# Kernel tuning notes

Measured on AMD Instinct MI355X. Metric: run time of the kernel, lower is better.

The kernel has to match this reference:

```python
import jax, jax.numpy as jnp
import numpy as np

V, E, HID, L = 32000, 2048, 8192, 4
H, KV, DK, DH = 16, 4, 128, 128
SEQ, WINDOW = 2048, 1024
EPS = 1e-5


def rms_norm(x):
    return x * jax.lax.rsqrt(jnp.mean(x * x, axis=-1, keepdims=True) + EPS)


def rope_buffers(seq_len, key_size):
    half = key_size // 2
    offset = jnp.arange(key_size) % half
    scales = jnp.power(10000.0, -2.0 / key_size * offset.astype(jnp.float32))
    angles = jnp.arange(seq_len, dtype=jnp.float32)[:, None] * scales[None, :]  # [S, DK]
    cos = jnp.cos(angles)
    sin = jnp.sin(angles)
    sin = sin.at[:, :half].multiply(-1.0)
    return cos, sin


def rotate(f, cos, sin):
    # f: [B, heads, S, DK]; cos/sin: [S, DK]
    half = DK // 2
    swapped = jnp.concatenate([f[..., half:], f[..., :half]], axis=-1)
    return cos * f + sin * swapped


def sliding_window_attention(q, k, v, window):
    # q: [B,H,S,DK], k: [B,KV,S,DK], v: [B,KV,S,DH]; GQA broadcast
    B, _, S, _ = q.shape
    G = H // KV
    qg = q.reshape(B, KV, G, S, DK)
    scores = jnp.einsum('bkgqd,bkjd->bkgqj', qg, k) / jnp.sqrt(jnp.asarray(DK, q.dtype))
    i = jnp.arange(S)[:, None]
    j = jnp.arange(S)[None, :]
    mask = (j <= i) & (i - j < window)
    scores = jnp.where(mask, scores, jnp.asarray(-1e9, scores.dtype))
    probs = jax.nn.softmax(scores, axis=-1)
    out = jnp.einsum('bkgqj,bkjd->bkgqd', probs, v)
    return out.reshape(B, H, S, DH)


def setup_inputs() -> dict:
    key = jax.random.key(0)
    ks = jax.random.split(key, 9)
    s = lambda k, shape, fan: jax.random.normal(k, shape, jnp.float32) / np.sqrt(fan)
    return {
        'tokens': jax.random.randint(ks[0], (1, SEQ), 0, V),
        'table': jax.random.normal(ks[1], (V, E), jnp.float32) * 0.02,
        'wq': s(ks[2], (L, E, H * DK), E),
        'wk': s(ks[3], (L, E, KV * DK), E),
        'wv': s(ks[4], (L, E, KV * DH), E),
        'wo': s(ks[5], (L, H * DH, E), H * DH),
        'w_up': s(ks[6], (L, E, 2 * HID), E),
        'w_down': s(ks[7], (L, HID, E), HID),
        'w_vocab': s(ks[8], (E, V), E),
    }


def reference(tokens, table, wq, wk, wv, wo, w_up, w_down, w_vocab):
    B, S = tokens.shape
    table = table.at[0].set(0.0)  # forward zeroes row 0 each call
    cos, sin = rope_buffers(S, DK)
    x = table[tokens]  # [B, S, E]
    for l in range(L):
        # --- self attention ---
        n = rms_norm(x)
        q = (n @ wq[l]).reshape(B, S, H, DK).transpose(0, 2, 1, 3)
        k = (n @ wk[l]).reshape(B, S, KV, DK).transpose(0, 2, 1, 3)
        v = (n @ wv[l]).reshape(B, S, KV, DH).transpose(0, 2, 1, 3)
        q = rotate(q, cos, sin)
        k = rotate(k, cos, sin)
        attn = sliding_window_attention(q, k, v, WINDOW)
        attn = attn.transpose(0, 2, 1, 3).reshape(B, S, H * DH)
        x = x + attn @ wo[l]
        # --- SwiGLU FFN ---
        n = rms_norm(x)
        gu = n @ w_up[l]
        gate, up = gu[..., :HID], gu[..., HID:]
        x = x + (up * jax.nn.silu(gate)) @ w_down[l]
    x = rms_norm(x)
    logits = x @ w_vocab  # [B, S, V]
    return logits
```

## Files before the change

### kernel.cpp

```cpp
#include <hip/hip_runtime.h>
#include <cstdint>

typedef unsigned short bf16u;
typedef __attribute__((ext_vector_type(8))) short short8;
typedef __attribute__((ext_vector_type(4))) float f32x4;

#define SEQ   2048
#define EMB   2048
#define NHEAD 16
#define NKV   4
#define DKH   128
#define HIDN  8192
#define NVOC  32000
#define NLAY  4
#define WIN   1024
#define QKV_N 3072

__device__ __forceinline__ bf16u f2bf(float f) {
  union { float f; uint32_t u; } v; v.f = f;
  uint32_t r = v.u + 0x7FFFu + ((v.u >> 16) & 1u);
  return (bf16u)(r >> 16);
}

__device__ __forceinline__ void gl2lds16(const void* g, void* l) {
  __builtin_amdgcn_global_load_lds(
      (const __attribute__((address_space(1))) void*)g,
      (__attribute__((address_space(3))) void*)l, 16, 0, 0);
}

__global__ __launch_bounds__(256) void embed_kernel(const int* __restrict__ tokens,
                                                    const float* __restrict__ table,
                                                    float* __restrict__ x) {
  int s = blockIdx.x;
  int tok = tokens[s];
  int i0 = threadIdx.x * 8;
  float4 a = {0,0,0,0}, b = {0,0,0,0};
  if (tok != 0) {
    const float* src = table + (size_t)tok * EMB;
    a = *(const float4*)(src + i0);
    b = *(const float4*)(src + i0 + 4);
  }
  *(float4*)(x + (size_t)s * EMB + i0) = a;
  *(float4*)(x + (size_t)s * EMB + i0 + 4) = b;
}

__global__ __launch_bounds__(256) void rmsnorm_kernel(const float* __restrict__ x,
                                                      bf16u* __restrict__ out) {
  int s = blockIdx.x;
  const float* row = x + (size_t)s * EMB;
  int i0 = threadIdx.x * 8;
  float4 a = *(const float4*)(row + i0);
  float4 b = *(const float4*)(row + i0 + 4);
  float ss = a.x*a.x + a.y*a.y + a.z*a.z + a.w*a.w
           + b.x*b.x + b.y*b.y + b.z*b.z + b.w*b.w;
  #pragma unroll
  for (int off = 1; off < 64; off <<= 1) ss += __shfl_xor(ss, off);
  __shared__ float red[4];
  if ((threadIdx.x & 63) == 0) red[threadIdx.x >> 6] = ss;
  __syncthreads();
  float scale = rsqrtf((red[0] + red[1] + red[2] + red[3]) * (1.0f / EMB) + 1e-5f);
  float v[8] = {a.x, a.y, a.z, a.w, b.x, b.y, b.z, b.w};
  short8 o;
  #pragma unroll
  for (int j = 0; j < 8; ++j) o[j] = (short)f2bf(v[j] * scale);
  *(short8*)(out + (size_t)s * EMB + i0) = o;
}

__global__ __launch_bounds__(256) void transp_kernel(const float* __restrict__ in,
                                                     bf16u* __restrict__ out,
                                                     int R, int C) {
  __shared__ float tile[32][33];
  int c0 = blockIdx.x * 32, r0 = blockIdx.y * 32;
  int tx = threadIdx.x & 31, ty = threadIdx.x >> 5;
  #pragma unroll
  for (int i = 0; i < 4; ++i)
    tile[ty + i * 8][tx] = in[(size_t)(r0 + ty + i * 8) * C + c0 + tx];
  __syncthreads();
  #pragma unroll
  for (int i = 0; i < 4; ++i)
    out[(size_t)(c0 + ty + i * 8) * R + r0 + tx] = f2bf(tile[tx][ty + i * 8]);
}

__global__ __launch_bounds__(256) void rope_kernel(const float* __restrict__ qkv,
                                                   bf16u* __restrict__ out, int col0) {
  int idx = blockIdx.x * 256 + threadIdx.x;
  int d = idx & 63;
  int s = (idx >> 6) & (SEQ - 1);
  int h = idx >> 17;
  const float* row = qkv + (size_t)s * QKV_N + col0 + h * DKH;
  float ang = (float)s * __powf(10000.0f, -(float)d * (1.0f / 64.0f));
  float si, c;
  sincosf(ang, &si, &c);
  float f0 = row[d], f1 = row[d + 64];
  bf16u* orow = out + ((size_t)h * SEQ + s) * DKH;
  orow[d]      = f2bf(c * f0 - si * f1);
  orow[d + 64] = f2bf(c * f1 + si * f0);
}

__global__ __launch_bounds__(256) void vconv_kernel(const float* __restrict__ qkv,
                                                    bf16u* __restrict__ vout) {
  int idx = blockIdx.x * 256 + threadIdx.x;
  int d = idx & 127;
  int kv = (idx >> 7) & 3;
  int s = idx >> 9;
  vout[((size_t)kv * SEQ + s) * DKH + d] = f2bf(qkv[(size_t)s * QKV_N + 2560 + kv * DKH + d]);
}

__global__ __launch_bounds__(256) void swiglu_kernel(const float* __restrict__ gu,
                                                     bf16u* __restrict__ h) {
  size_t idx = (size_t)blockIdx.x * 256 + threadIdx.x;
  int s = (int)(idx >> 13);
  int j = (int)(idx & 8191);
  float g = gu[(size_t)s * 16384 + j];
  float u = gu[(size_t)s * 16384 + 8192 + j];
  float sil = g / (1.0f + __expf(-g));
  h[idx] = f2bf(u * sil);
}

__global__ __launch_bounds__(256) void reduce4_kernel(float* __restrict__ x,
                                                      const float* __restrict__ p) {
  size_t i = ((size_t)blockIdx.x * 256 + threadIdx.x) * 4;
  const size_t MN = (size_t)SEQ * EMB;
  float4 a = *(const float4*)(x + i);
  float4 b0 = *(const float4*)(p + i);
  float4 b1 = *(const float4*)(p + i + MN);
  float4 b2 = *(const float4*)(p + i + 2 * MN);
  float4 b3 = *(const float4*)(p + i + 3 * MN);
  a.x += b0.x + b1.x + b2.x + b3.x;
  a.y += b0.y + b1.y + b2.y + b3.y;
  a.z += b0.z + b1.z + b2.z + b3.z;
  a.w += b0.w + b1.w + b2.w + b3.w;
  *(float4*)(x + i) = a;
}

template <int MODE>
__global__ __launch_bounds__(256) void gemm_kernel(const bf16u* __restrict__ A,
                                                   const bf16u* __restrict__ Bt,
                                                   void* __restrict__ C,
                                                   int M, int N, int K) {
  __shared__ __align__(16) char lds[2][2][8192];

  int nx = gridDim.x, ny = gridDim.y;
  int nwg = nx * ny;
  int orig = blockIdx.y * nx + blockIdx.x;
  int q = nwg >> 3, r = nwg & 7;
  int xcd = orig & 7, loc = orig >> 3;
  int id = (xcd < r ? xcd * (q + 1) : r * (q + 1) + (xcd - r) * q) + loc;
  int bx = id / ny, by = id - bx * ny;
  int n0 = bx * 128, m0 = by * 128;

  int t = threadIdx.x;
  int w = t >> 6, l = t & 63;
  int wm = (w >> 1) * 64, wn = (w & 1) * 64;
  int l15 = l & 15, l4 = l >> 4;

  int srow = w * 16 + (l >> 2);
  int scol = (l & 3) * 8;

  f32x4 acc[4][4] = {};

  auto stage = [&](int buf, int k0) {
    #pragma unroll
    for (int i = 0; i < 2; ++i) {
      gl2lds16(A  + (size_t)(m0 + i * 64 + srow) * K + k0 + scol,
               &lds[buf][0][i * 4096 + w * 1024]);
      gl2lds16(Bt + (size_t)(n0 + i * 64 + srow) * K + k0 + scol,
               &lds[buf][1][i * 4096 + w * 1024]);
    }
  };

  auto compute = [&](int buf) {
    short8 af[4], bfr[4];
    #pragma unroll
    for (int i = 0; i < 4; ++i) {
      af[i]  = *(const short8*)(&lds[buf][0][((wm + i * 16 + l15) * 32 + l4 * 8) * 2]);
      bfr[i] = *(const short8*)(&lds[buf][1][((wn + i * 16 + l15) * 32 + l4 * 8) * 2]);
    }
    #pragma unroll
    for (int i = 0; i < 4; ++i)
      #pragma unroll
      for (int j = 0; j < 4; ++j)
        acc[i][j] = __builtin_amdgcn_mfma_f32_16x16x32_bf16(af[i], bfr[j], acc[i][j], 0, 0, 0);
  };

  int nt = K >> 5;
  int cur = 0;
  stage(0, 0);
  __syncthreads();
  for (int tt = 0; tt < nt; ++tt) {
    if (tt + 1 < nt) stage(cur ^ 1, (tt + 1) * 32);
    compute(cur);
    __syncthreads();
    cur ^= 1;
  }

  #pragma unroll
  for (int i = 0; i < 4; ++i)
    #pragma unroll
    for (int j = 0; j < 4; ++j) {
      int col = n0 + wn + j * 16 + l15;
      #pragma unroll
      for (int rr = 0; rr < 4; ++rr) {
        int row = m0 + wm + i * 16 + l4 * 4 + rr;
        float v = acc[i][j][rr];
        if (MODE == 0) {
          ((bf16u*)C)[(size_t)row * N + col] = f2bf(v);
        } else if (MODE == 1) {
          float* p = (float*)C + (size_t)row * N + col;
          *p += v;
        } else {
          ((float*)C)[(size_t)row * N + col] = v;
        }
      }
    }
}

__device__ __forceinline__ void stage_half(const bf16u* __restrict__ p, int ld,
                                           int row0, int k0, char* slotBase, int t) {
  int r  = t >> 3, c8 = t & 7;
  int cs = (c8 ^ (r & 7)) << 3;
  gl2lds16(p + (size_t)(row0 + r) * ld + k0 + cs, slotBase + t * 16);
  gl2lds16(p + (size_t)(row0 + 64 + r) * ld + k0 + cs, slotBase + 8192 + t * 16);
}

template<int KK>
__device__ __forceinline__ short8 read_frag(const char* slot, int row, int l4) {
  int kc = KK * 4 + l4;
  return *(const short8*)(slot + row * 128 + ((kc ^ (row & 7)) << 4));
}

template<int NH>
__device__ __forceinline__ void mfma_quad(f32x4 (&acc)[8][4], const short8 (&a)[8],
                                          short8 b0, short8 b1) {
  __builtin_amdgcn_s_setprio(1);
  #pragma unroll
  for (int mi = 0; mi < 8; ++mi) {
    acc[mi][NH * 2]     = __builtin_amdgcn_mfma_f32_16x16x32_bf16(a[mi], b0, acc[mi][NH * 2], 0, 0, 0);
    acc[mi][NH * 2 + 1] = __builtin_amdgcn_mfma_f32_16x16x32_bf16(a[mi], b1, acc[mi][NH * 2 + 1], 0, 0, 0);
  }
  __builtin_amdgcn_s_setprio(0);
}

template <int MODE>
__global__ __launch_bounds__(512) void gemm256_kernel(const bf16u* __restrict__ A,
                                                      const bf16u* __restrict__ Bt,
                                                      void* __restrict__ C,
                                                      int M, int N, int K, int ldk) {
  __shared__ __align__(16) char lds[131072];

  int koff = blockIdx.z * K;
  A  += koff;
  Bt += koff;
  float* Cz = (float*)C + (size_t)blockIdx.z * M * N;

  int nx = gridDim.x, ny = gridDim.y;
  int nwg = nx * ny;
  int orig = blockIdx.y * nx + blockIdx.x;
  int q8 = nwg >> 3, r8 = nwg & 7;
  int xcd = orig & 7, loc = orig >> 3;
  int id = (xcd < r8 ? xcd * (q8 + 1) : r8 * (q8 + 1) + (xcd - r8) * q8) + loc;
  int bx = id / ny, by = id - bx * ny;
  int n0 = bx * 256, m0 = by * 256;

  int t = threadIdx.x;
  int wid = t >> 6, lane = t & 63;
  int wr = wid >> 2, wc = wid & 3, bh = wc >> 1;
  int l15 = lane & 15, l4 = lane >> 4;

  char* AS0 = lds;              char* AS1 = lds + 16384;
  char* AS2 = lds + 32768;      char* AS3 = lds + 49152;
  char* BS0 = lds + 65536;      char* BS1 = lds + 81920;
  char* BS2 = lds + 98304;      char* BS3 = lds + 114688;

  const char* ASe = lds + wr * 16384;
  const char* ASo = ASe + 32768;
  const char* BSe = lds + 65536 + bh * 16384;
  const char* BSo = BSe + 32768;

  int brow = (wc & 1) * 64;

  f32x4 acc[8][4] = {};
  short8 a[8];
  short8 b0, b1;

  int NT = K >> 6;
  int NI = NT >> 1;

  stage_half(A,  ldk, m0,       0,  AS0, t);
  stage_half(A,  ldk, m0 + 128, 0,  AS1, t);
  stage_half(Bt, ldk, n0,       0,  BS0, t);
  stage_half(Bt, ldk, n0 + 128, 0,  BS1, t);
  stage_half(A,  ldk, m0,       64, AS2, t);
  asm volatile("s_waitcnt vmcnt(2)" ::: "memory");
  __builtin_amdgcn_s_barrier();
  __builtin_amdgcn_sched_barrier(0);

  for (int I = 0; I < NI; ++I) {
    int t0k = I * 128;
    int t1k = t0k + 64;
    bool notlast = (I + 1 < NI);

    #pragma unroll
    for (int mi = 0; mi < 8; ++mi) a[mi] = read_frag<0>(ASe, mi * 16 + l15, l4);
    b0 = read_frag<0>(BSe, brow + l15, l4);
    b1 = read_frag<0>(BSe, brow + 16 + l15, l4);
    stage_half(A, ldk, m0 + 128, t1k, AS3, t);
    __builtin_amdgcn_s_barrier();
    mfma_quad<0>(acc, a, b0, b1);
    __builtin_amdgcn_s_barrier();

    b0 = read_frag<0>(BSe, brow + 32 + l15, l4);
    b1 = read_frag<0>(BSe, brow + 48 + l15, l4);
    stage_half(Bt, ldk, n0, t1k, BS2, t);
    __builtin_amdgcn_s_barrier();
    mfma_quad<1>(acc, a, b0, b1);
    __builtin_amdgcn_s_barrier();

    #pragma unroll
    for (int mi = 0; mi < 8; ++mi) a[mi] = read_frag<1>(ASe, mi * 16 + l15, l4);
    b0 = read_frag<1>(BSe, brow + l15, l4);
    b1 = read_frag<1>(BSe, brow + 16 + l15, l4);
    stage_half(Bt, ldk, n0 + 128, t1k, BS3, t);
    __builtin_amdgcn_s_barrier();
    mfma_quad<0>(acc, a, b0, b1);
    __builtin_amdgcn_s_barrier();

    b0 = read_frag<1>(BSe, brow + 32 + l15, l4);
    b1 = read_frag<1>(BSe, brow + 48 + l15, l4);
    if (notlast) stage_half(A, ldk, m0, t0k + 128, AS0, t);
    if (notlast) { asm volatile("s_waitcnt vmcnt(2)" ::: "memory"); }
    else         { asm volatile("s_waitcnt vmcnt(0)" ::: "memory"); }
    __builtin_amdgcn_s_barrier();
    __builtin_amdgcn_sched_barrier(0);
    mfma_quad<1>(acc, a, b0, b1);
    __builtin_amdgcn_s_barrier();

    #pragma unroll
    for (int mi = 0; mi < 8; ++mi) a[mi] = read_frag<0>(ASo, mi * 16 + l15, l4);
    b0 = read_frag<0>(BSo, brow + l15, l4);
    b1 = read_frag<0>(BSo, brow + 16 + l15, l4);
    if (notlast) stage_half(A, ldk, m0 + 128, t0k + 128, AS1, t);
    __builtin_amdgcn_s_barrier();
    mfma_quad<0>(acc, a, b0, b1);
    __builtin_amdgcn_s_barrier();

    b0 = read_frag<0>(BSo, brow + 32 + l15, l4);
    b1 = read_frag<0>(BSo, brow + 48 + l15, l4);
    if (notlast) stage_half(Bt, ldk, n0, t0k + 128, BS0, t);
    __builtin_amdgcn_s_barrier();
    mfma_quad<1>(acc, a, b0, b1);
    __builtin_amdgcn_s_barrier();

    #pragma unroll
    for (int mi = 0; mi < 8; ++mi) a[mi] = read_frag<1>(ASo, mi * 16 + l15, l4);
    b0 = read_frag<1>(BSo, brow + l15, l4);
    b1 = read_frag<1>(BSo, brow + 16 + l15, l4);
    if (notlast) stage_half(Bt, ldk, n0 + 128, t0k + 128, BS1, t);
    __builtin_amdgcn_s_barrier();
    mfma_quad<0>(acc, a, b0, b1);
    __builtin_amdgcn_s_barrier();

    b0 = read_frag<1>(BSo, brow + 32 + l15, l4);
    b1 = read_frag<1>(BSo, brow + 48 + l15, l4);
    if (notlast) {
      stage_half(A, ldk, m0, t0k + 192, AS2, t);
      asm volatile("s_waitcnt vmcnt(2)" ::: "memory");
    }
    __builtin_amdgcn_s_barrier();
    __builtin_amdgcn_sched_barrier(0);
    mfma_quad<1>(acc, a, b0, b1);
    __builtin_amdgcn_s_barrier();
  }

  #pragma unroll
  for (int mi = 0; mi < 8; ++mi)
    #pragma unroll
    for (int ni = 0; ni < 4; ++ni) {
      int col = n0 + wc * 64 + ni * 16 + l15;
      #pragma unroll
      for (int rr = 0; rr < 4; ++rr) {
        int row = m0 + wr * 128 + mi * 16 + l4 * 4 + rr;
        float v = acc[mi][ni][rr];
        if (MODE == 0) {
          ((bf16u*)C)[(size_t)row * N + col] = f2bf(v);
        } else if (MODE == 1) {
          float* p = (float*)C + (size_t)row * N + col;
          *p += v;
        } else {
          Cz[(size_t)row * N + col] = v;
        }
      }
    }
}

__global__ __launch_bounds__(256) void attn_kernel(const bf16u* __restrict__ q_bf,
                                                   const bf16u* __restrict__ k_bf,
                                                   const bf16u* __restrict__ v_bf,
                                                   bf16u* __restrict__ attn_out) {
  int h = blockIdx.y;
  int q0 = blockIdx.x * 64;
  int kvh = h >> 2;
  const bf16u* Kp = k_bf + (size_t)kvh * SEQ * DKH;
  const bf16u* Vp = v_bf + (size_t)kvh * SEQ * DKH;

  __shared__ __align__(16) char  Klds[32 * 128 * 2];
  __shared__ __align__(16) bf16u Vlds[128][40];
  __shared__ __align__(16) bf16u Plds[4][16][40];

  int t = threadIdx.x, wave = t >> 6, lane = t & 63;
  int l15 = lane & 15, l4 = lane >> 4;
  int qrow0 = q0 + wave * 16;

  short8 qf[4];
  #pragma unroll
  for (int ks = 0; ks < 4; ++ks)
    qf[ks] = *(const short8*)(q_bf + ((size_t)h * SEQ + qrow0 + l15) * DKH + ks * 32 + l4 * 8);

  f32x4 o[8] = {};
  float m[4], lsum[4];
  #pragma unroll
  for (int r = 0; r < 4; ++r) { m[r] = -INFINITY; lsum[r] = 0.0f; }

  int jstart = q0 >= (WIN - 1) ? ((q0 - (WIN - 1)) & ~31) : 0;

  for (int j0 = jstart; j0 < q0 + 64; j0 += 32) {
    __syncthreads();
    #pragma unroll
    for (int i = 0; i < 2; ++i) {
      int c = t + i * 256;
      int key = c >> 4, cc = c & 15;
      int off = key * 256 + cc * 16; off ^= (key & 7) << 4;
      *(short8*)(Klds + off) = *(const short8*)(Kp + (size_t)(j0 + key) * DKH + cc * 8);
    }
    {
      int key = t >> 3, d0 = (t & 7) * 16;
      const bf16u* src = Vp + (size_t)(j0 + key) * DKH + d0;
      #pragma unroll
      for (int i = 0; i < 16; ++i) Vlds[d0 + i][key] = src[i];
    }
    __syncthreads();

    f32x4 sacc[2] = {};
    #pragma unroll
    for (int nt = 0; nt < 2; ++nt) {
      int key = nt * 16 + l15;
      #pragma unroll
      for (int ks = 0; ks < 4; ++ks) {
        int off = key * 256 + ks * 64 + l4 * 16; off ^= (key & 7) << 4;
        short8 kf = *(short8*)(Klds + off);
        sacc[nt] = __builtin_amdgcn_mfma_f32_16x16x32_bf16(qf[ks], kf, sacc[nt], 0, 0, 0);
      }
    }

    float sv[2][4];
    #pragma unroll
    for (int nt = 0; nt < 2; ++nt) {
      int jk = j0 + nt * 16 + l15;
      #pragma unroll
      for (int r = 0; r < 4; ++r) {
        int iq = qrow0 + l4 * 4 + r;
        float s = sacc[nt][r] * 0.08838834764831845f;
        bool valid = (jk <= iq) && (iq - jk < WIN);
        sv[nt][r] = valid ? s : -1e9f;
      }
    }

    float p[2][4];
    #pragma unroll
    for (int r = 0; r < 4; ++r) {
      float mx = fmaxf(sv[0][r], sv[1][r]);
      #pragma unroll
      for (int off = 1; off < 16; off <<= 1) mx = fmaxf(mx, __shfl_xor(mx, off));
      float mn = fmaxf(m[r], mx);
      float alpha = __expf(m[r] - mn);
      p[0][r] = __expf(sv[0][r] - mn);
      p[1][r] = __expf(sv[1][r] - mn);
      float ps = p[0][r] + p[1][r];
      #pragma unroll
      for (int off = 1; off < 16; off <<= 1) ps += __shfl_xor(ps, off);
      lsum[r] = lsum[r] * alpha + ps;
      m[r] = mn;
      #pragma unroll
      for (int d = 0; d < 8; ++d) o[d][r] *= alpha;
    }

    #pragma unroll
    for (int nt = 0; nt < 2; ++nt)
      #pragma unroll
      for (int r = 0; r < 4; ++r)
        Plds[wave][l4 * 4 + r][nt * 16 + l15] = f2bf(p[nt][r]);

    short8 pf = *(short8*)(&Plds[wave][l15][l4 * 8]);
    #pragma unroll
    for (int d = 0; d < 8; ++d) {
      short8 vf = *(short8*)(&Vlds[d * 16 + l15][l4 * 8]);
      o[d] = __builtin_amdgcn_mfma_f32_16x16x32_bf16(pf, vf, o[d], 0, 0, 0);
    }
  }

  #pragma unroll
  for (int d = 0; d < 8; ++d)
    #pragma unroll
    for (int r = 0; r < 4; ++r) {
      int row = qrow0 + l4 * 4 + r;
      attn_out[(size_t)row * (NHEAD * DKH) + h * DKH + d * 16 + l15] = f2bf(o[d][r] / lsum[r]);
    }
}

extern "C" void kernel_launch(void* const* d_in, const int* in_sizes, int n_in,
                              void* d_out, int out_size, void* d_ws, size_t ws_size,
                              hipStream_t stream) {
  const int*   tokens  = (const int*)d_in[0];
  const float* table   = (const float*)d_in[1];
  const float* wq      = (const float*)d_in[2];
  const float* wk      = (const float*)d_in[3];
  const float* wv      = (const float*)d_in[4];
  const float* wo      = (const float*)d_in[5];
  const float* w_up    = (const float*)d_in[6];
  const float* w_down  = (const float*)d_in[7];
  const float* w_vocab = (const float*)d_in[8];
  float* out = (float*)d_out;

  char* base = (char*)d_ws;
  size_t o = 0;
  auto alloc = [&](size_t bytes) { size_t r = o; o += (bytes + 255) & ~(size_t)255; return r; };
  size_t o_x     = alloc((size_t)SEQ * EMB * 4);
  size_t o_nbf   = alloc((size_t)SEQ * EMB * 2);
  size_t o_qkvw  = alloc((size_t)QKV_N * EMB * 2);
  size_t o_wot   = alloc((size_t)EMB * EMB * 2);
  size_t o_wupt  = alloc((size_t)2 * HIDN * EMB * 2);
  size_t o_wdnt  = alloc((size_t)EMB * HIDN * 2);
  size_t o_qkvf  = alloc((size_t)SEQ * QKV_N * 4);
  size_t o_qbf   = alloc((size_t)NHEAD * SEQ * DKH * 2);
  size_t o_kbf   = alloc((size_t)NKV * SEQ * DKH * 2);
  size_t o_vbf   = alloc((size_t)NKV * SEQ * DKH * 2);
  size_t o_attn  = alloc((size_t)SEQ * EMB * 2);
  size_t o_guf   = alloc((size_t)SEQ * 2 * HIDN * 4);
  size_t o_hbf   = alloc((size_t)SEQ * HIDN * 2);
  size_t o_wvoct = o_guf;

  float* x      = (float*)(base + o_x);
  bf16u* n_bf   = (bf16u*)(base + o_nbf);
  bf16u* qkvw_t = (bf16u*)(base + o_qkvw);
  bf16u* wo_t   = (bf16u*)(base + o_wot);
  bf16u* wup_t  = (bf16u*)(base + o_wupt);
  bf16u* wdn_t  = (bf16u*)(base + o_wdnt);
  float* qkv_f  = (float*)(base + o_qkvf);
  bf16u* q_bf   = (bf16u*)(base + o_qbf);
  bf16u* k_bf   = (bf16u*)(base + o_kbf);
  bf16u* v_bf   = (bf16u*)(base + o_vbf);
  bf16u* attn_b = (bf16u*)(base + o_attn);
  float* gu_f   = (float*)(base + o_guf);
  float* part   = (float*)(base + o_guf);
  bf16u* h_bf   = (bf16u*)(base + o_hbf);
  bf16u* wvoc_t = (bf16u*)(base + o_wvoct);

  embed_kernel<<<SEQ, 256, 0, stream>>>(tokens, table, x);

  for (int l = 0; l < NLAY; ++l) {
    transp_kernel<<<dim3(EMB / 32, EMB / 32), 256, 0, stream>>>(
        wq + (size_t)l * EMB * EMB, qkvw_t, EMB, EMB);
    transp_kernel<<<dim3(512 / 32, EMB / 32), 256, 0, stream>>>(
        wk + (size_t)l * EMB * 512, qkvw_t + (size_t)2048 * EMB, EMB, 512);
    transp_kernel<<<dim3(512 / 32, EMB / 32), 256, 0, stream>>>(
        wv + (size_t)l * EMB * 512, qkvw_t + (size_t)2560 * EMB, EMB, 512);
    transp_kernel<<<dim3(EMB / 32, EMB / 32), 256, 0, stream>>>(
        wo + (size_t)l * EMB * EMB, wo_t, EMB, EMB);
    transp_kernel<<<dim3(2 * HIDN / 32, EMB / 32), 256, 0, stream>>>(
        w_up + (size_t)l * EMB * 2 * HIDN, wup_t, EMB, 2 * HIDN);
    transp_kernel<<<dim3(EMB / 32, HIDN / 32), 256, 0, stream>>>(
        w_down + (size_t)l * HIDN * EMB, wdn_t, HIDN, EMB);

    rmsnorm_kernel<<<SEQ, 256, 0, stream>>>(x, n_bf);
    gemm_kernel<2><<<dim3(QKV_N / 128, SEQ / 128), 256, 0, stream>>>(
        n_bf, qkvw_t, qkv_f, SEQ, QKV_N, EMB);

    rope_kernel<<<NHEAD * SEQ * 64 / 256, 256, 0, stream>>>(qkv_f, q_bf, 0);
    rope_kernel<<<NKV * SEQ * 64 / 256, 256, 0, stream>>>(qkv_f, k_bf, 2048);
    vconv_kernel<<<NKV * SEQ * 128 / 256, 256, 0, stream>>>(qkv_f, v_bf);

    attn_kernel<<<dim3(SEQ / 64, NHEAD), 256, 0, stream>>>(q_bf, k_bf, v_bf, attn_b);

    gemm_kernel<1><<<dim3(EMB / 128, SEQ / 128), 256, 0, stream>>>(
        attn_b, wo_t, x, SEQ, EMB, EMB);

    rmsnorm_kernel<<<SEQ, 256, 0, stream>>>(x, n_bf);
    gemm256_kernel<2><<<dim3(2 * HIDN / 256, SEQ / 256), 512, 0, stream>>>(
        n_bf, wup_t, gu_f, SEQ, 2 * HIDN, EMB, EMB);
    swiglu_kernel<<<SEQ * HIDN / 256, 256, 0, stream>>>(gu_f, h_bf);
    gemm256_kernel<2><<<dim3(EMB / 256, SEQ / 256, 4), 512, 0, stream>>>(
        h_bf, wdn_t, part, SEQ, EMB, 2048, HIDN);
    reduce4_kernel<<<SEQ * EMB / 1024, 256, 0, stream>>>(x, part);
  }

  transp_kernel<<<dim3(NVOC / 32, EMB / 32), 256, 0, stream>>>(w_vocab, wvoc_t, EMB, NVOC);
  rmsnorm_kernel<<<SEQ, 256, 0, stream>>>(x, n_bf);
  gemm256_kernel<2><<<dim3(NVOC / 256, SEQ / 256), 512, 0, stream>>>(
      n_bf, wvoc_t, out, SEQ, NVOC, EMB, EMB);
}
```

Measured before the change: 2.688 ms.

## Fuse SwiGLU into up-projection epilogue and widen attention key tiles

The up-projection weight columns are interleaved (gate, up) during transpose so the GEMM epilogue can pair neighbouring lanes via shuffle and write the SwiGLU output directly in bf16. This removes the fp32 gate/up intermediate and the separate swiglu pass. The attention kernel now processes 64 keys per iteration instead of 32 and only rescales the running max when it grows by more than a threshold, which cuts the number of barriers and exponentials. In exchange, LDS use per block goes up, and the lazy rescale adds a small numeric-range risk.

```diff
diff --git a/kernel.cpp b/kernel.cpp
--- a/kernel.cpp
+++ b/kernel.cpp
@@ -68,7 +68,7 @@
 
 __global__ __launch_bounds__(256) void transp_kernel(const float* __restrict__ in,
                                                      bf16u* __restrict__ out,
-                                                     int R, int C) {
+                                                     int R, int C, int pairhalf) {
   __shared__ float tile[32][33];
   int c0 = blockIdx.x * 32, r0 = blockIdx.y * 32;
   int tx = threadIdx.x & 31, ty = threadIdx.x >> 5;
@@ -77,8 +77,11 @@
     tile[ty + i * 8][tx] = in[(size_t)(r0 + ty + i * 8) * C + c0 + tx];
   __syncthreads();
   #pragma unroll
-  for (int i = 0; i < 4; ++i)
-    out[(size_t)(c0 + ty + i * 8) * R + r0 + tx] = f2bf(tile[tx][ty + i * 8]);
+  for (int i = 0; i < 4; ++i) {
+    int c = c0 + ty + i * 8;
+    int n = pairhalf ? (c < pairhalf ? 2 * c : 2 * (c - pairhalf) + 1) : c;
+    out[(size_t)n * R + r0 + tx] = f2bf(tile[tx][ty + i * 8]);
+  }
 }
 
 __global__ __launch_bounds__(256) void rope_kernel(const float* __restrict__ qkv,
@@ -106,17 +109,6 @@
   vout[((size_t)kv * SEQ + s) * DKH + d] = f2bf(qkv[(size_t)s * QKV_N + 2560 + kv * DKH + d]);
 }
 
-__global__ __launch_bounds__(256) void swiglu_kernel(const float* __restrict__ gu,
-                                                     bf16u* __restrict__ h) {
-  size_t idx = (size_t)blockIdx.x * 256 + threadIdx.x;
-  int s = (int)(idx >> 13);
-  int j = (int)(idx & 8191);
-  float g = gu[(size_t)s * 16384 + j];
-  float u = gu[(size_t)s * 16384 + 8192 + j];
-  float sil = g / (1.0f + __expf(-g));
-  h[idx] = f2bf(u * sil);
-}
-
 __global__ __launch_bounds__(256) void reduce4_kernel(float* __restrict__ x,
                                                       const float* __restrict__ p) {
   size_t i = ((size_t)blockIdx.x * 256 + threadIdx.x) * 4;
@@ -381,13 +373,19 @@
       for (int rr = 0; rr < 4; ++rr) {
         int row = m0 + wr * 128 + mi * 16 + l4 * 4 + rr;
         float v = acc[mi][ni][rr];
-        if (MODE == 0) {
-          ((bf16u*)C)[(size_t)row * N + col] = f2bf(v);
+        if (MODE == 3) {
+          float pv = __shfl_xor(v, 1);
+          if ((l15 & 1) == 0) {
+            float hval = pv * (v / (1.0f + __expf(-v)));
+            ((bf16u*)C)[(size_t)row * HIDN + (col >> 1)] = f2bf(hval);
+          }
+        } else if (MODE == 2) {
+          Cz[(size_t)row * N + col] = v;
         } else if (MODE == 1) {
           float* p = (float*)C + (size_t)row * N + col;
           *p += v;
         } else {
-          Cz[(size_t)row * N + col] = v;
+          ((bf16u*)C)[(size_t)row * N + col] = f2bf(v);
         }
       }
     }
@@ -403,9 +401,9 @@
   const bf16u* Kp = k_bf + (size_t)kvh * SEQ * DKH;
   const bf16u* Vp = v_bf + (size_t)kvh * SEQ * DKH;
 
-  __shared__ __align__(16) char  Klds[32 * 128 * 2];
-  __shared__ __align__(16) bf16u Vlds[128][40];
-  __shared__ __align__(16) bf16u Plds[4][16][40];
+  __shared__ __align__(16) char  Klds[64 * 128 * 2];
+  __shared__ __align__(16) bf16u Vlds[128][72];
+  __shared__ __align__(16) bf16u Plds[4][16][72];
 
   int t = threadIdx.x, wave = t >> 6, lane = t & 63;
   int l15 = lane & 15, l4 = lane >> 4;
@@ -421,28 +419,29 @@
   #pragma unroll
   for (int r = 0; r < 4; ++r) { m[r] = -INFINITY; lsum[r] = 0.0f; }
 
-  int jstart = q0 >= (WIN - 1) ? ((q0 - (WIN - 1)) & ~31) : 0;
-
-  for (int j0 = jstart; j0 < q0 + 64; j0 += 32) {
+  int jstart = q0 >= WIN ? ((q0 - (WIN - 1)) & ~63) : 0;
+
+  for (int j0 = jstart; j0 < q0 + 64; j0 += 64) {
     __syncthreads();
     #pragma unroll
-    for (int i = 0; i < 2; ++i) {
+    for (int i = 0; i < 4; ++i) {
       int c = t + i * 256;
       int key = c >> 4, cc = c & 15;
       int off = key * 256 + cc * 16; off ^= (key & 7) << 4;
       *(short8*)(Klds + off) = *(const short8*)(Kp + (size_t)(j0 + key) * DKH + cc * 8);
     }
-    {
-      int key = t >> 3, d0 = (t & 7) * 16;
+    #pragma unroll
+    for (int hh = 0; hh < 2; ++hh) {
+      int key = hh * 32 + (t >> 3), d0 = (t & 7) * 16;
       const bf16u* src = Vp + (size_t)(j0 + key) * DKH + d0;
       #pragma unroll
       for (int i = 0; i < 16; ++i) Vlds[d0 + i][key] = src[i];
     }
     __syncthreads();
 
-    f32x4 sacc[2] = {};
-    #pragma unroll
-    for (int nt = 0; nt < 2; ++nt) {
+    f32x4 sacc[4] = {};
+    #pragma unroll
+    for (int nt = 0; nt < 4; ++nt) {
       int key = nt * 16 + l15;
       #pragma unroll
       for (int ks = 0; ks < 4; ++ks) {
@@ -452,9 +451,9 @@
       }
     }
 
-    float sv[2][4];
-    #pragma unroll
-    for (int nt = 0; nt < 2; ++nt) {
+    float sv[4][4];
+    #pragma unroll
+    for (int nt = 0; nt < 4; ++nt) {
       int jk = j0 + nt * 16 + l15;
       #pragma unroll
       for (int r = 0; r < 4; ++r) {
@@ -465,36 +464,54 @@
       }
     }
 
-    float p[2][4];
+    float mxr[4];
     #pragma unroll
     for (int r = 0; r < 4; ++r) {
-      float mx = fmaxf(sv[0][r], sv[1][r]);
+      float mx = fmaxf(fmaxf(sv[0][r], sv[1][r]), fmaxf(sv[2][r], sv[3][r]));
       #pragma unroll
       for (int off = 1; off < 16; off <<= 1) mx = fmaxf(mx, __shfl_xor(mx, off));
-      float mn = fmaxf(m[r], mx);
-      float alpha = __expf(m[r] - mn);
-      p[0][r] = __expf(sv[0][r] - mn);
-      p[1][r] = __expf(sv[1][r] - mn);
-      float ps = p[0][r] + p[1][r];
+      mxr[r] = mx;
+    }
+
+    bool grow = (mxr[0] > m[0] + 8.0f) || (mxr[1] > m[1] + 8.0f) ||
+                (mxr[2] > m[2] + 8.0f) || (mxr[3] > m[3] + 8.0f);
+    if (__any(grow)) {
+      #pragma unroll
+      for (int r = 0; r < 4; ++r) {
+        float mn = fmaxf(m[r], mxr[r]);
+        float alpha = __expf(m[r] - mn);
+        m[r] = mn;
+        lsum[r] *= alpha;
+        #pragma unroll
+        for (int d = 0; d < 8; ++d) o[d][r] *= alpha;
+      }
+    }
+
+    float p[4][4];
+    #pragma unroll
+    for (int r = 0; r < 4; ++r) {
+      float ps = 0.0f;
+      #pragma unroll
+      for (int nt = 0; nt < 4; ++nt) { p[nt][r] = __expf(sv[nt][r] - m[r]); ps += p[nt][r]; }
       #pragma unroll
       for (int off = 1; off < 16; off <<= 1) ps += __shfl_xor(ps, off);
-      lsum[r] = lsum[r] * alpha + ps;
-      m[r] = mn;
-      #pragma unroll
-      for (int d = 0; d < 8; ++d) o[d][r] *= alpha;
-    }
-
-    #pragma unroll
-    for (int nt = 0; nt < 2; ++nt)
+      lsum[r] += ps;
+    }
+
+    #pragma unroll
+    for (int nt = 0; nt < 4; ++nt)
       #pragma unroll
       for (int r = 0; r < 4; ++r)
         Plds[wave][l4 * 4 + r][nt * 16 + l15] = f2bf(p[nt][r]);
 
-    short8 pf = *(short8*)(&Plds[wave][l15][l4 * 8]);
-    #pragma unroll
-    for (int d = 0; d < 8; ++d) {
-      short8 vf = *(short8*)(&Vlds[d * 16 + l15][l4 * 8]);
-      o[d] = __builtin_amdgcn_mfma_f32_16x16x32_bf16(pf, vf, o[d], 0, 0, 0);
+    #pragma unroll
+    for (int kk = 0; kk < 2; ++kk) {
+      short8 pf = *(short8*)(&Plds[wave][l15][kk * 32 + l4 * 8]);
+      #pragma unroll
+      for (int d = 0; d < 8; ++d) {
+        short8 vf = *(short8*)(&Vlds[d * 16 + l15][kk * 32 + l4 * 8]);
+        o[d] = __builtin_amdgcn_mfma_f32_16x16x32_bf16(pf, vf, o[d], 0, 0, 0);
+      }
     }
   }
 
@@ -535,9 +552,8 @@
   size_t o_kbf   = alloc((size_t)NKV * SEQ * DKH * 2);
   size_t o_vbf   = alloc((size_t)NKV * SEQ * DKH * 2);
   size_t o_attn  = alloc((size_t)SEQ * EMB * 2);
-  size_t o_guf   = alloc((size_t)SEQ * 2 * HIDN * 4);
+  size_t o_big   = alloc((size_t)SEQ * 2 * HIDN * 4);
   size_t o_hbf   = alloc((size_t)SEQ * HIDN * 2);
-  size_t o_wvoct = o_guf;
 
   float* x      = (float*)(base + o_x);
   bf16u* n_bf   = (bf16u*)(base + o_nbf);
@@ -550,26 +566,25 @@
   bf16u* k_bf   = (bf16u*)(base + o_kbf);
   bf16u* v_bf   = (bf16u*)(base + o_vbf);
   bf16u* attn_b = (bf16u*)(base + o_attn);
-  float* gu_f   = (float*)(base + o_guf);
-  float* part   = (float*)(base + o_guf);
+  float* part   = (float*)(base + o_big);
   bf16u* h_bf   = (bf16u*)(base + o_hbf);
-  bf16u* wvoc_t = (bf16u*)(base + o_wvoct);
+  bf16u* wvoc_t = (bf16u*)(base + o_big);
 
   embed_kernel<<<SEQ, 256, 0, stream>>>(tokens, table, x);
 
   for (int l = 0; l < NLAY; ++l) {
     transp_kernel<<<dim3(EMB / 32, EMB / 32), 256, 0, stream>>>(
-        wq + (size_t)l * EMB * EMB, qkvw_t, EMB, EMB);
+        wq + (size_t)l * EMB * EMB, qkvw_t, EMB, EMB, 0);
     transp_kernel<<<dim3(512 / 32, EMB / 32), 256, 0, stream>>>(
-        wk + (size_t)l * EMB * 512, qkvw_t + (size_t)2048 * EMB, EMB, 512);
+        wk + (size_t)l * EMB * 512, qkvw_t + (size_t)2048 * EMB, EMB, 512, 0);
     transp_kernel<<<dim3(512 / 32, EMB / 32), 256, 0, stream>>>(
-        wv + (size_t)l * EMB * 512, qkvw_t + (size_t)2560 * EMB, EMB, 512);
+        wv + (size_t)l * EMB * 512, qkvw_t + (size_t)2560 * EMB, EMB, 512, 0);
     transp_kernel<<<dim3(EMB / 32, EMB / 32), 256, 0, stream>>>(
-        wo + (size_t)l * EMB * EMB, wo_t, EMB, EMB);
+        wo + (size_t)l * EMB * EMB, wo_t, EMB, EMB, 0);
     transp_kernel<<<dim3(2 * HIDN / 32, EMB / 32), 256, 0, stream>>>(
-        w_up + (size_t)l * EMB * 2 * HIDN, wup_t, EMB, 2 * HIDN);
+        w_up + (size_t)l * EMB * 2 * HIDN, wup_t, EMB, 2 * HIDN, HIDN);
     transp_kernel<<<dim3(EMB / 32, HIDN / 32), 256, 0, stream>>>(
-        w_down + (size_t)l * HIDN * EMB, wdn_t, HIDN, EMB);
+        w_down + (size_t)l * HIDN * EMB, wdn_t, HIDN, EMB, 0);
 
     rmsnorm_kernel<<<SEQ, 256, 0, stream>>>(x, n_bf);
     gemm_kernel<2><<<dim3(QKV_N / 128, SEQ / 128), 256, 0, stream>>>(
@@ -585,15 +600,14 @@
         attn_b, wo_t, x, SEQ, EMB, EMB);
 
     rmsnorm_kernel<<<SEQ, 256, 0, stream>>>(x, n_bf);
-    gemm256_kernel<2><<<dim3(2 * HIDN / 256, SEQ / 256), 512, 0, stream>>>(
-        n_bf, wup_t, gu_f, SEQ, 2 * HIDN, EMB, EMB);
-    swiglu_kernel<<<SEQ * HIDN / 256, 256, 0, stream>>>(gu_f, h_bf);
+    gemm256_kernel<3><<<dim3(2 * HIDN / 256, SEQ / 256), 512, 0, stream>>>(
+        n_bf, wup_t, h_bf, SEQ, 2 * HIDN, EMB, EMB);
     gemm256_kernel<2><<<dim3(EMB / 256, SEQ / 256, 4), 512, 0, stream>>>(
         h_bf, wdn_t, part, SEQ, EMB, 2048, HIDN);
     reduce4_kernel<<<SEQ * EMB / 1024, 256, 0, stream>>>(x, part);
   }
 
-  transp_kernel<<<dim3(NVOC / 32, EMB / 32), 256, 0, stream>>>(w_vocab, wvoc_t, EMB, NVOC);
+  transp_kernel<<<dim3(NVOC / 32, EMB / 32), 256, 0, stream>>>(w_vocab, wvoc_t, EMB, NVOC, 0);
   rmsnorm_kernel<<<SEQ, 256, 0, stream>>>(x, n_bf);
   gemm256_kernel<2><<<dim3(NVOC / 256, SEQ / 256), 512, 0, stream>>>(
       n_bf, wvoc_t, out, SEQ, NVOC, EMB, EMB);
```

Measured after the change: 2.505 ms. -6.8%, faster.
